# Kernel optimization log

Hardware: AMD Instinct MI355X
Metric: run time of the kernel (lower is better)

The kernel has to match this reference:

```python
import jax, jax.numpy as jnp
import numpy as np

N, L, S, D, H = 4, 8192, 8192, 256, 8
HD = D // H
EPS_ATTN = 1e-6
EPS_LN = 1e-5


def _layer_norm(x, g, b):
    mu = jnp.mean(x, axis=-1, keepdims=True)
    var = jnp.mean((x - mu) ** 2, axis=-1, keepdims=True)
    return (x - mu) / jnp.sqrt(var + EPS_LN) * g + b


def setup_inputs() -> dict:
    key = jax.random.key(0)
    ks = jax.random.split(key, 12)
    sc = 1.0 / np.sqrt(D)
    sc2 = 1.0 / np.sqrt(2 * D)
    return {
        "x": jax.random.normal(ks[0], (N, L, D), jnp.float32),
        "source": jax.random.normal(ks[1], (N, S, D), jnp.float32),
        "x_mask": jnp.ones((N, L), jnp.float32),
        "source_mask": jnp.ones((N, S), jnp.float32),
        "Wq": jax.random.normal(ks[2], (D, D), jnp.float32) * sc,
        "Wk": jax.random.normal(ks[3], (D, D), jnp.float32) * sc,
        "Wv": jax.random.normal(ks[4], (D, D), jnp.float32) * sc,
        "Wm": jax.random.normal(ks[5], (D, D), jnp.float32) * sc,
        "W1": jax.random.normal(ks[6], (2 * D, 2 * D), jnp.float32) * sc2,
        "W2": jax.random.normal(ks[7], (D, 2 * D), jnp.float32) * sc2,
        "g1": jnp.ones((D,), jnp.float32),
        "b1": jnp.zeros((D,), jnp.float32),
        "g2": jnp.ones((D,), jnp.float32),
        "b2": jnp.zeros((D,), jnp.float32),
    }


def reference(x, source, x_mask, source_mask, Wq, Wk, Wv, Wm, W1, W2, g1, b1, g2, b2):
    n = x.shape[0]
    # QKV projections (Linear without bias: y = x @ W.T), split into heads
    q = (x @ Wq.T).reshape(n, -1, H, HD)         # [N, L, H, HD]
    k = (source @ Wk.T).reshape(n, -1, H, HD)    # [N, S, H, HD]
    v = (source @ Wv.T).reshape(n, -1, H, HD)    # [N, S, H, HD]

    # kernelized linear attention: phi(x) = elu(x) + 1
    Q = jax.nn.elu(q) + 1.0
    K = jax.nn.elu(k) + 1.0
    Q = Q * x_mask[:, :, None, None]
    K = K * source_mask[:, :, None, None]
    v = v * source_mask[:, :, None, None]

    s_len = v.shape[1]
    v = v / s_len
    KV = jnp.einsum('nshd,nshv->nhdv', K, v)                       # [N, H, HD, HD]
    Z = 1.0 / (jnp.einsum('nlhd,nhd->nlh', Q, K.sum(axis=1)) + EPS_ATTN)
    msg = jnp.einsum('nlhd,nhdv,nlh->nlhv', Q, KV, Z) * s_len      # [N, L, H, HD]

    # merge heads + LN
    msg = msg.reshape(n, -1, H * HD) @ Wm.T
    msg = _layer_norm(msg, g1, b1)

    # concat-MLP + LN + residual
    h = jnp.concatenate([x, msg], axis=2) @ W1.T
    h = jax.nn.relu(h) @ W2.T
    h = _layer_norm(h, g2, b2)
    return x + h
```

## Files before the change

### kernel.cpp

```cpp
#include <hip/hip_runtime.h>

using short8 = __attribute__((ext_vector_type(8))) short;
using f32x4  = __attribute__((ext_vector_type(4))) float;

__device__ __forceinline__ float bf2f(unsigned short u) {
  union { unsigned int i; float f; } c; c.i = ((unsigned int)u) << 16; return c.f;
}
__device__ __forceinline__ unsigned short f2bf(float x) {
  union { float f; unsigned int i; } c; c.f = x;
  unsigned int r = c.i + 0x7fffu + ((c.i >> 16) & 1u);
  return (unsigned short)(r >> 16);
}

__global__ void cast_all(const float* __restrict__ x, const float* __restrict__ src,
                         const float* __restrict__ wq, const float* __restrict__ wk,
                         const float* __restrict__ wv, const float* __restrict__ wm,
                         const float* __restrict__ w1, const float* __restrict__ w2,
                         unsigned short* __restrict__ xb, unsigned short* __restrict__ sb,
                         unsigned short* __restrict__ Wb) {
  const int NV = 2097152;
  int stride = gridDim.x * blockDim.x;
  for (int i = blockIdx.x * blockDim.x + threadIdx.x; i < 2 * NV + 163840; i += stride) {
    const float4* s; ushort4* d; int j;
    if (i < NV)            { s = (const float4*)x;   d = (ushort4*)xb; j = i; }
    else if (i < 2 * NV)   { s = (const float4*)src; d = (ushort4*)sb; j = i - NV; }
    else {
      j = i - 2 * NV;
      d = (ushort4*)Wb;
      const float* w;
      int off;
      if      (j < 16384)  { w = wq; off = j; }
      else if (j < 32768)  { w = wk; off = j - 16384; }
      else if (j < 49152)  { w = wv; off = j - 32768; }
      else if (j < 65536)  { w = wm; off = j - 49152; }
      else if (j < 131072) { w = w1; off = j - 65536; }
      else                 { w = w2; off = j - 131072; }
      float4 v = ((const float4*)w)[off];
      ushort4 o; o.x = f2bf(v.x); o.y = f2bf(v.y); o.z = f2bf(v.z); o.w = f2bf(v.w);
      d[j] = o;
      continue;
    }
    float4 v = s[j];
    ushort4 o; o.x = f2bf(v.x); o.y = f2bf(v.y); o.z = f2bf(v.z); o.w = f2bf(v.w);
    d[j] = o;
  }
}

enum { EPI_ELU1_MASK = 1, EPI_KV = 2, EPI_RELU_BF16 = 3 };

template<int EPI, bool SPLITA>
__global__ __launch_bounds__(256)
void gemm_nt(const unsigned short* __restrict__ A, const unsigned short* __restrict__ A2,
             const unsigned short* __restrict__ B,
             void* __restrict__ C0, void* __restrict__ C1, const float* __restrict__ aux,
             int M, int O, int K, float scale) {
  __shared__ unsigned short As[128 * 64];
  __shared__ unsigned short Bs[128 * 64];
  const int t  = threadIdx.x;
  const int w  = t >> 6, l = t & 63;
  const int wr = w >> 1, wc = w & 1;
  const int lr = l & 15, kg = l >> 4;
  const int brow = blockIdx.x * 128, bcol = blockIdx.y * 128;
  const int rsub = l >> 3;
  const int swz  = 8 * ((l & 7) ^ rsub);

  f32x4 acc[4][4];
  f32x4 zero = {0.f, 0.f, 0.f, 0.f};
  #pragma unroll
  for (int m = 0; m < 4; m++)
    #pragma unroll
    for (int n = 0; n < 4; n++) acc[m][n] = zero;

  for (int k0 = 0; k0 < K; k0 += 64) {
    #pragma unroll
    for (int i = 0; i < 4; i++) {
      int c = w * 4 + i;
      int row = c * 8 + rsub;
      const unsigned short* ga;
      if (SPLITA) {
        const unsigned short* base = (k0 < 256) ? A : A2;
        ga = base + (size_t)(brow + row) * 256 + (k0 & 255) + swz;
      } else {
        ga = A + (size_t)(brow + row) * K + k0 + swz;
      }
      const unsigned short* gb = B + (size_t)(bcol + row) * K + k0 + swz;
      __builtin_amdgcn_global_load_lds((__attribute__((address_space(1))) unsigned int*)ga,
          (__attribute__((address_space(3))) unsigned int*)(As + c * 512), 16, 0, 0);
      __builtin_amdgcn_global_load_lds((__attribute__((address_space(1))) unsigned int*)gb,
          (__attribute__((address_space(3))) unsigned int*)(Bs + c * 512), 16, 0, 0);
    }
    __syncthreads();
    #pragma unroll
    for (int kk = 0; kk < 2; kk++) {
      short8 af[4], bfr[4];
      #pragma unroll
      for (int m = 0; m < 4; m++) {
        int r = wr * 64 + m * 16 + lr;
        int cb = kk * 64 + kg * 16;
        af[m] = *(const short8*)((const char*)As + r * 128 + (cb ^ ((r & 7) << 4)));
      }
      #pragma unroll
      for (int n = 0; n < 4; n++) {
        int r = wc * 64 + n * 16 + lr;
        int cb = kk * 64 + kg * 16;
        bfr[n] = *(const short8*)((const char*)Bs + r * 128 + (cb ^ ((r & 7) << 4)));
      }
      #pragma unroll
      for (int m = 0; m < 4; m++)
        #pragma unroll
        for (int n = 0; n < 4; n++)
          acc[m][n] = __builtin_amdgcn_mfma_f32_16x16x32_bf16(af[m], bfr[n], acc[m][n], 0, 0, 0);
    }
    __syncthreads();
  }

  #pragma unroll
  for (int m = 0; m < 4; m++) {
    #pragma unroll
    for (int n = 0; n < 4; n++) {
      int col = bcol + wc * 64 + n * 16 + lr;
      #pragma unroll
      for (int j = 0; j < 4; j++) {
        int row = brow + wr * 64 + m * 16 + kg * 4 + j;
        float v = acc[m][n][j];
        if (EPI == EPI_ELU1_MASK) {
          float e = v > 0.f ? v + 1.f : __expf(v);
          ((unsigned short*)C0)[(size_t)row * O + col] = f2bf(e * aux[row]);
        } else if (EPI == EPI_KV) {
          int colm = col & 255;
          if (col < 256) {
            float e = v > 0.f ? v + 1.f : __expf(v);
            ((unsigned short*)C0)[(size_t)row * 256 + colm] = f2bf(e * aux[row]);
          } else {
            ((unsigned short*)C1)[(size_t)row * 256 + colm] = f2bf(v * aux[row] * scale);
          }
        } else {
          ((unsigned short*)C0)[(size_t)row * O + col] = f2bf(v > 0.f ? v : 0.f);
        }
      }
    }
  }
}

template<int MODE>
__global__ __launch_bounds__(512)
void gemm_ln(const unsigned short* __restrict__ A, const unsigned short* __restrict__ B,
             void* __restrict__ Cout, const float* __restrict__ g, const float* __restrict__ b,
             const float* __restrict__ xres, int K) {
  __shared__ unsigned short As[128 * 64];
  __shared__ unsigned short Bs[256 * 64];
  __shared__ float lnsum[128][4];
  __shared__ float lnsq[128][4];
  const int t  = threadIdx.x;
  const int w  = t >> 6, l = t & 63;
  const int wr = w >> 2, wc = w & 3;
  const int lr = l & 15, kg = l >> 4;
  const int brow = blockIdx.x * 128;
  const int rsub = l >> 3;
  const int swz  = 8 * ((l & 7) ^ rsub);

  f32x4 acc[4][4];
  f32x4 zero = {0.f, 0.f, 0.f, 0.f};
  #pragma unroll
  for (int m = 0; m < 4; m++)
    #pragma unroll
    for (int n = 0; n < 4; n++) acc[m][n] = zero;

  for (int k0 = 0; k0 < K; k0 += 64) {
    #pragma unroll
    for (int i = 0; i < 6; i++) {
      int c = w * 6 + i;
      if (c < 16) {
        int row = c * 8 + rsub;
        const unsigned short* ga = A + (size_t)(brow + row) * K + k0 + swz;
        __builtin_amdgcn_global_load_lds((__attribute__((address_space(1))) unsigned int*)ga,
            (__attribute__((address_space(3))) unsigned int*)(As + c * 512), 16, 0, 0);
      } else {
        int row = (c - 16) * 8 + rsub;
        const unsigned short* gb = B + (size_t)row * K + k0 + swz;
        __builtin_amdgcn_global_load_lds((__attribute__((address_space(1))) unsigned int*)gb,
            (__attribute__((address_space(3))) unsigned int*)(Bs + (c - 16) * 512), 16, 0, 0);
      }
    }
    __syncthreads();
    #pragma unroll
    for (int kk = 0; kk < 2; kk++) {
      short8 af[4], bfr[4];
      #pragma unroll
      for (int m = 0; m < 4; m++) {
        int r = wr * 64 + m * 16 + lr;
        int cb = kk * 64 + kg * 16;
        af[m] = *(const short8*)((const char*)As + r * 128 + (cb ^ ((r & 7) << 4)));
      }
      #pragma unroll
      for (int n = 0; n < 4; n++) {
        int r = wc * 64 + n * 16 + lr;
        int cb = kk * 64 + kg * 16;
        bfr[n] = *(const short8*)((const char*)Bs + r * 128 + (cb ^ ((r & 7) << 4)));
      }
      #pragma unroll
      for (int m = 0; m < 4; m++)
        #pragma unroll
        for (int n = 0; n < 4; n++)
          acc[m][n] = __builtin_amdgcn_mfma_f32_16x16x32_bf16(af[m], bfr[n], acc[m][n], 0, 0, 0);
    }
    __syncthreads();
  }

  #pragma unroll
  for (int m = 0; m < 4; m++) {
    #pragma unroll
    for (int j = 0; j < 4; j++) {
      int rl = wr * 64 + m * 16 + kg * 4 + j;
      float s = 0.f, qq = 0.f;
      #pragma unroll
      for (int n = 0; n < 4; n++) { float v = acc[m][n][j]; s += v; qq += v * v; }
      #pragma unroll
      for (int off = 1; off < 16; off <<= 1) {
        s  += __shfl_xor(s, off, 64);
        qq += __shfl_xor(qq, off, 64);
      }
      if (lr == 0) { lnsum[rl][wc] = s; lnsq[rl][wc] = qq; }
    }
  }
  __syncthreads();

  float gl[4], bl[4];
  #pragma unroll
  for (int n = 0; n < 4; n++) {
    int col = wc * 64 + n * 16 + lr;
    gl[n] = g[col]; bl[n] = b[col];
  }
  #pragma unroll
  for (int m = 0; m < 4; m++) {
    #pragma unroll
    for (int j = 0; j < 4; j++) {
      int rl = wr * 64 + m * 16 + kg * 4 + j;
      float s  = lnsum[rl][0] + lnsum[rl][1] + lnsum[rl][2] + lnsum[rl][3];
      float qq = lnsq[rl][0] + lnsq[rl][1] + lnsq[rl][2] + lnsq[rl][3];
      float mu = s * (1.f / 256.f);
      float var = qq * (1.f / 256.f) - mu * mu;
      float rs = rsqrtf(var + 1e-5f);
      size_t row = (size_t)brow + rl;
      #pragma unroll
      for (int n = 0; n < 4; n++) {
        int col = wc * 64 + n * 16 + lr;
        float y = (acc[m][n][j] - mu) * rs * gl[n] + bl[n];
        if (MODE == 0) ((unsigned short*)Cout)[row * 256 + col] = f2bf(y);
        else           ((float*)Cout)[row * 256 + col] = xres[row * 256 + col] + y;
      }
    }
  }
}

__global__ __launch_bounds__(1024)
void kv_partial(const unsigned short* __restrict__ Kb, const unsigned short* __restrict__ Vb,
                float* __restrict__ part_kv, float* __restrict__ part_ks) {
  __shared__ float Ks[16][256];
  __shared__ float Vs[16][256];
  const int t   = threadIdx.x;
  const int blk = blockIdx.x;
  const int n   = blk >> 6;
  const int s0  = (blk & 63) * 128;
  const int h   = t >> 7, g = (t >> 5) & 3, dv = t & 31;
  const int r16 = t >> 6, c4 = (t & 63) * 4;
  const int cbase = h * 32;
  f32x4 acc0 = {0.f, 0.f, 0.f, 0.f}, acc1 = {0.f, 0.f, 0.f, 0.f};
  float ks = 0.f;

  for (int tile = 0; tile < 8; ++tile) {
    int s = s0 + tile * 16;
    size_t gbase = ((size_t)(n * 8192 + s + r16)) * 256 + c4;
    ushort4 kk = *(const ushort4*)&Kb[gbase];
    ushort4 vv = *(const ushort4*)&Vb[gbase];
    __syncthreads();
    float4 kf; kf.x = bf2f(kk.x); kf.y = bf2f(kk.y); kf.z = bf2f(kk.z); kf.w = bf2f(kk.w);
    float4 vf; vf.x = bf2f(vv.x); vf.y = bf2f(vv.y); vf.z = bf2f(vv.z); vf.w = bf2f(vv.w);
    *(float4*)&Ks[r16][c4] = kf;
    *(float4*)&Vs[r16][c4] = vf;
    __syncthreads();
    if (t < 256) {
      #pragma unroll
      for (int r = 0; r < 16; ++r) ks += Ks[r][t];
    }
    #pragma unroll
    for (int si = 0; si < 16; ++si) {
      f32x4 k0 = *(const f32x4*)&Ks[si][cbase + g * 8];
      f32x4 k1 = *(const f32x4*)&Ks[si][cbase + g * 8 + 4];
      float vx = Vs[si][cbase + dv];
      acc0 += k0 * vx;
      acc1 += k1 * vx;
    }
  }
  float* dst = &part_kv[(size_t)blk * 8192 + h * 1024 + dv * 32 + g * 8];
  *(float4*)(dst + 0) = *(float4*)&acc0;
  *(float4*)(dst + 4) = *(float4*)&acc1;
  if (t < 256) part_ks[blk * 256 + t] = ks;
}

__global__ __launch_bounds__(1024)
void kv_finalize(const float* __restrict__ part_kv, const float* __restrict__ part_ks,
                 float* __restrict__ KVt, float* __restrict__ Ksum) {
  const int b = blockIdx.x, t = threadIdx.x;
  if (b < 32) {
    int n = b >> 3;
    int e = (b & 7) * 1024 + t;
    const float* p = part_kv + (size_t)n * 64 * 8192 + e;
    float s = 0.f;
    #pragma unroll 8
    for (int c = 0; c < 64; ++c) s += p[(size_t)c * 8192];
    KVt[(size_t)n * 8192 + e] = s;
  } else {
    int n = b - 32;
    if (t < 256) {
      const float* p = part_ks + n * 64 * 256 + t;
      float s = 0.f;
      #pragma unroll 8
      for (int c = 0; c < 64; ++c) s += p[c * 256];
      Ksum[n * 256 + t] = s;
    }
  }
}

__global__ __launch_bounds__(256)
void msg_apply(const unsigned short* __restrict__ Qb, const float* __restrict__ KVt,
               const float* __restrict__ Ksum, unsigned short* __restrict__ Mb) {
  __shared__ float KVs[8192];
  __shared__ float Kss[256];
  const int t = threadIdx.x;
  const int row0 = blockIdx.x * 32;
  const int n = blockIdx.x >> 8;
  const int r = t >> 3, h = t & 7;
  for (int i = t; i < 8192; i += 256) {
    int j = i ^ (((i >> 10) & 7) << 2);
    KVs[j] = KVt[(size_t)n * 8192 + i];
  }
  Kss[t] = Ksum[n * 256 + t];
  __syncthreads();

  const unsigned short* qp = &Qb[(size_t)(row0 + r) * 256 + h * 32];
  float q[32];
  #pragma unroll
  for (int i = 0; i < 4; ++i) {
    short8 v = *(const short8*)(qp + i * 8);
    #pragma unroll
    for (int j = 0; j < 8; ++j) q[i * 8 + j] = bf2f((unsigned short)v[j]);
  }
  float zden = 0.f;
  #pragma unroll
  for (int sl = 0; sl < 8; ++sl) {
    f32x4 kv = *(const f32x4*)&Kss[h * 32 + sl * 4];
    zden += q[sl*4+0]*kv[0] + q[sl*4+1]*kv[1] + q[sl*4+2]*kv[2] + q[sl*4+3]*kv[3];
  }
  float z = 8192.f / (zden + 1e-6f);
  const int kvbase = h * 1024;
  short8 ov[4];
  #pragma unroll
  for (int dv = 0; dv < 32; ++dv) {
    float o = 0.f;
    #pragma unroll
    for (int sl = 0; sl < 8; ++sl) {
      f32x4 kv = *(const f32x4*)&KVs[kvbase + dv * 32 + ((sl ^ h) << 2)];
      o += q[sl*4+0]*kv[0] + q[sl*4+1]*kv[1] + q[sl*4+2]*kv[2] + q[sl*4+3]*kv[3];
    }
    ov[dv >> 3][dv & 7] = (short)f2bf(o * z);
  }
  unsigned short* op = (unsigned short*)&Mb[(size_t)(row0 + r) * 256 + h * 32];
  #pragma unroll
  for (int i = 0; i < 4; ++i) *(short8*)(op + i * 8) = ov[i];
}

extern "C" void kernel_launch(void* const* d_in, const int* in_sizes, int n_in,
                              void* d_out, int out_size, void* d_ws, size_t ws_size,
                              hipStream_t stream) {
  const float* x   = (const float*)d_in[0];
  const float* src = (const float*)d_in[1];
  const float* xm  = (const float*)d_in[2];
  const float* sm  = (const float*)d_in[3];
  const float* Wq  = (const float*)d_in[4];
  const float* Wk  = (const float*)d_in[5];
  const float* Wv  = (const float*)d_in[6];
  const float* Wm  = (const float*)d_in[7];
  const float* W1  = (const float*)d_in[8];
  const float* W2  = (const float*)d_in[9];
  const float* g1  = (const float*)d_in[10];
  const float* b1  = (const float*)d_in[11];
  const float* g2  = (const float*)d_in[12];
  const float* b2  = (const float*)d_in[13];
  float* out = (float*)d_out;
  char*  ws  = (char*)d_ws;

  unsigned short* xb   = (unsigned short*)(ws);
  unsigned short* sb   = (unsigned short*)(ws + 16777216);
  unsigned short* Qb   = (unsigned short*)(ws + 33554432);
  unsigned short* Mb   = (unsigned short*)(ws + 50331648);
  unsigned short* Kb   = (unsigned short*)(ws + 67108864);
  unsigned short* Vb   = (unsigned short*)(ws + 83886080);
  float*          pkv  = (float*)(ws + 16777216);
  float*          pks  = (float*)(ws + 16777216 + 8388608);
  unsigned short* msgb = (unsigned short*)(ws + 67108864);
  unsigned short* h1b  = (unsigned short*)(ws + 33554432);
  float*          KV   = (float*)(ws + 100663296);
  float*          Ksm  = (float*)(ws + 100663296 + 131072);
  unsigned short* Wb   = (unsigned short*)(ws + 100663296 + 135168);
  unsigned short* Wqb = Wb;
  unsigned short* Wkb = Wb + 65536;
  unsigned short* Wmb = Wb + 196608;
  unsigned short* W1b = Wb + 262144;
  unsigned short* W2b = Wb + 524288;

  cast_all<<<4096, 256, 0, stream>>>(x, src, Wq, Wk, Wv, Wm, W1, W2, xb, sb, Wb);

  gemm_nt<EPI_ELU1_MASK, false><<<dim3(256, 2), 256, 0, stream>>>(
      xb, nullptr, Wqb, (void*)Qb, nullptr, xm, 32768, 256, 256, 0.f);
  gemm_nt<EPI_KV, false><<<dim3(256, 4), 256, 0, stream>>>(
      sb, nullptr, Wkb, (void*)Kb, (void*)Vb, sm, 32768, 512, 256, 1.f / 8192.f);

  kv_partial<<<256, 1024, 0, stream>>>(Kb, Vb, pkv, pks);
  kv_finalize<<<36, 1024, 0, stream>>>(pkv, pks, KV, Ksm);
  msg_apply<<<1024, 256, 0, stream>>>(Qb, KV, Ksm, Mb);

  gemm_ln<0><<<256, 512, 0, stream>>>(Mb, Wmb, (void*)msgb, g1, b1, nullptr, 256);

  gemm_nt<EPI_RELU_BF16, true><<<dim3(256, 4), 256, 0, stream>>>(
      xb, msgb, W1b, (void*)h1b, nullptr, nullptr, 32768, 512, 512, 0.f);

  gemm_ln<1><<<256, 512, 0, stream>>>(h1b, W2b, (void*)out, g2, b2, x, 512);
}
```

Measured before the change: 286.5 us.

## Merge Q and KV projection GEMMs and double-buffer LDS tiles

Combines the Q projection and the K/V projection into a single GEMM launch with a six-column-tile grid, choosing x or source as the A operand per column block and writing Q, K, V in the epilogue. Adds double-buffered shared memory so the next K-slice is prefetched asynchronously while MFMAs run on the current one. This aims to cut launch overhead and tail effects and to hide global load latency, at the cost of doubling LDS use, which may lower occupancy.

```diff
diff --git a/kernel.cpp b/kernel.cpp
--- a/kernel.cpp
+++ b/kernel.cpp
@@ -46,16 +46,17 @@
   }
 }
 
-enum { EPI_ELU1_MASK = 1, EPI_KV = 2, EPI_RELU_BF16 = 3 };
-
-template<int EPI, bool SPLITA>
+enum { EPI_QKV = 0, EPI_RELU_BF16 = 1 };
+
+template<int EPI, int ASEL>
 __global__ __launch_bounds__(256)
 void gemm_nt(const unsigned short* __restrict__ A, const unsigned short* __restrict__ A2,
              const unsigned short* __restrict__ B,
-             void* __restrict__ C0, void* __restrict__ C1, const float* __restrict__ aux,
+             void* __restrict__ C0, void* __restrict__ C1, void* __restrict__ C2,
+             const float* __restrict__ aux0, const float* __restrict__ aux1,
              int M, int O, int K, float scale) {
-  __shared__ unsigned short As[128 * 64];
-  __shared__ unsigned short Bs[128 * 64];
+  __shared__ unsigned short As[2][128 * 64];
+  __shared__ unsigned short Bs[2][128 * 64];
   const int t  = threadIdx.x;
   const int w  = t >> 6, l = t & 63;
   const int wr = w >> 1, wc = w & 1;
@@ -64,6 +65,8 @@
   const int rsub = l >> 3;
   const int swz  = 8 * ((l & 7) ^ rsub);
 
+  const unsigned short* Ablk = (ASEL == 2 && bcol >= 256) ? A2 : A;
+
   f32x4 acc[4][4];
   f32x4 zero = {0.f, 0.f, 0.f, 0.f};
   #pragma unroll
@@ -71,25 +74,31 @@
     #pragma unroll
     for (int n = 0; n < 4; n++) acc[m][n] = zero;
 
-  for (int k0 = 0; k0 < K; k0 += 64) {
+  auto STAGE = [&](int bufi, int k0s) {
     #pragma unroll
     for (int i = 0; i < 4; i++) {
       int c = w * 4 + i;
       int row = c * 8 + rsub;
       const unsigned short* ga;
-      if (SPLITA) {
-        const unsigned short* base = (k0 < 256) ? A : A2;
-        ga = base + (size_t)(brow + row) * 256 + (k0 & 255) + swz;
+      if (ASEL == 1) {
+        const unsigned short* base = (k0s < 256) ? A : A2;
+        ga = base + (size_t)(brow + row) * 256 + (k0s & 255) + swz;
       } else {
-        ga = A + (size_t)(brow + row) * K + k0 + swz;
-      }
-      const unsigned short* gb = B + (size_t)(bcol + row) * K + k0 + swz;
+        ga = Ablk + (size_t)(brow + row) * K + k0s + swz;
+      }
+      const unsigned short* gb = B + (size_t)(bcol + row) * K + k0s + swz;
       __builtin_amdgcn_global_load_lds((__attribute__((address_space(1))) unsigned int*)ga,
-          (__attribute__((address_space(3))) unsigned int*)(As + c * 512), 16, 0, 0);
+          (__attribute__((address_space(3))) unsigned int*)(&As[bufi][0] + c * 512), 16, 0, 0);
       __builtin_amdgcn_global_load_lds((__attribute__((address_space(1))) unsigned int*)gb,
-          (__attribute__((address_space(3))) unsigned int*)(Bs + c * 512), 16, 0, 0);
-    }
-    __syncthreads();
+          (__attribute__((address_space(3))) unsigned int*)(&Bs[bufi][0] + c * 512), 16, 0, 0);
+    }
+  };
+
+  STAGE(0, 0);
+  __syncthreads();
+  int cur = 0;
+  for (int k0 = 0; k0 < K; k0 += 64) {
+    if (k0 + 64 < K) STAGE(cur ^ 1, k0 + 64);
     #pragma unroll
     for (int kk = 0; kk < 2; kk++) {
       short8 af[4], bfr[4];
@@ -97,13 +106,13 @@
       for (int m = 0; m < 4; m++) {
         int r = wr * 64 + m * 16 + lr;
         int cb = kk * 64 + kg * 16;
-        af[m] = *(const short8*)((const char*)As + r * 128 + (cb ^ ((r & 7) << 4)));
+        af[m] = *(const short8*)((const char*)&As[cur][0] + r * 128 + (cb ^ ((r & 7) << 4)));
       }
       #pragma unroll
       for (int n = 0; n < 4; n++) {
         int r = wc * 64 + n * 16 + lr;
         int cb = kk * 64 + kg * 16;
-        bfr[n] = *(const short8*)((const char*)Bs + r * 128 + (cb ^ ((r & 7) << 4)));
+        bfr[n] = *(const short8*)((const char*)&Bs[cur][0] + r * 128 + (cb ^ ((r & 7) << 4)));
       }
       #pragma unroll
       for (int m = 0; m < 4; m++)
@@ -112,6 +121,7 @@
           acc[m][n] = __builtin_amdgcn_mfma_f32_16x16x32_bf16(af[m], bfr[n], acc[m][n], 0, 0, 0);
     }
     __syncthreads();
+    cur ^= 1;
   }
 
   #pragma unroll
@@ -123,16 +133,15 @@
       for (int j = 0; j < 4; j++) {
         int row = brow + wr * 64 + m * 16 + kg * 4 + j;
         float v = acc[m][n][j];
-        if (EPI == EPI_ELU1_MASK) {
-          float e = v > 0.f ? v + 1.f : __expf(v);
-          ((unsigned short*)C0)[(size_t)row * O + col] = f2bf(e * aux[row]);
-        } else if (EPI == EPI_KV) {
-          int colm = col & 255;
+        if (EPI == EPI_QKV) {
           if (col < 256) {
             float e = v > 0.f ? v + 1.f : __expf(v);
-            ((unsigned short*)C0)[(size_t)row * 256 + colm] = f2bf(e * aux[row]);
+            ((unsigned short*)C0)[(size_t)row * 256 + col] = f2bf(e * aux0[row]);
+          } else if (col < 512) {
+            float e = v > 0.f ? v + 1.f : __expf(v);
+            ((unsigned short*)C1)[(size_t)row * 256 + (col - 256)] = f2bf(e * aux1[row]);
           } else {
-            ((unsigned short*)C1)[(size_t)row * 256 + colm] = f2bf(v * aux[row] * scale);
+            ((unsigned short*)C2)[(size_t)row * 256 + (col - 512)] = f2bf(v * aux1[row] * scale);
           }
         } else {
           ((unsigned short*)C0)[(size_t)row * O + col] = f2bf(v > 0.f ? v : 0.f);
@@ -404,17 +413,14 @@
   float*          Ksm  = (float*)(ws + 100663296 + 131072);
   unsigned short* Wb   = (unsigned short*)(ws + 100663296 + 135168);
   unsigned short* Wqb = Wb;
-  unsigned short* Wkb = Wb + 65536;
   unsigned short* Wmb = Wb + 196608;
   unsigned short* W1b = Wb + 262144;
   unsigned short* W2b = Wb + 524288;
 
   cast_all<<<4096, 256, 0, stream>>>(x, src, Wq, Wk, Wv, Wm, W1, W2, xb, sb, Wb);
 
-  gemm_nt<EPI_ELU1_MASK, false><<<dim3(256, 2), 256, 0, stream>>>(
-      xb, nullptr, Wqb, (void*)Qb, nullptr, xm, 32768, 256, 256, 0.f);
-  gemm_nt<EPI_KV, false><<<dim3(256, 4), 256, 0, stream>>>(
-      sb, nullptr, Wkb, (void*)Kb, (void*)Vb, sm, 32768, 512, 256, 1.f / 8192.f);
+  gemm_nt<EPI_QKV, 2><<<dim3(256, 6), 256, 0, stream>>>(
+      xb, sb, Wqb, (void*)Qb, (void*)Kb, (void*)Vb, xm, sm, 32768, 768, 256, 1.f / 8192.f);
 
   kv_partial<<<256, 1024, 0, stream>>>(Kb, Vb, pkv, pks);
   kv_finalize<<<36, 1024, 0, stream>>>(pkv, pks, KV, Ksm);
@@ -422,8 +428,8 @@
 
   gemm_ln<0><<<256, 512, 0, stream>>>(Mb, Wmb, (void*)msgb, g1, b1, nullptr, 256);
 
-  gemm_nt<EPI_RELU_BF16, true><<<dim3(256, 4), 256, 0, stream>>>(
-      xb, msgb, W1b, (void*)h1b, nullptr, nullptr, 32768, 512, 512, 0.f);
+  gemm_nt<EPI_RELU_BF16, 1><<<dim3(256, 4), 256, 0, stream>>>(
+      xb, msgb, W1b, (void*)h1b, nullptr, nullptr, nullptr, nullptr, 32768, 512, 512, 0.f);
 
   gemm_ln<1><<<256, 512, 0, stream>>>(h1b, W2b, (void*)out, g2, b2, x, 512);
 }
```

New measurement: 299.3 us. +4.5%, slower.

## Merge Q and KV projections into one launch with wider 128x256 tiles

Applied to the files above, without the earlier changes.

The separate Q and K/V projection GEMMs become one launch with three 256-column panels: the Q panel reads x and the K and V panels read source. The GEMM kernel moves to 512 threads and 128x256 output tiles, for both the QKV and the W1 ReLU GEMM, so each A tile is reused across twice as many output columns. This removes one launch and halves redundant A-tile loads, at the cost of more LDS per block and fewer blocks, which may reduce occupancy.

```diff
diff --git a/kernel.cpp b/kernel.cpp
--- a/kernel.cpp
+++ b/kernel.cpp
@@ -46,24 +46,29 @@
   }
 }
 
-enum { EPI_ELU1_MASK = 1, EPI_KV = 2, EPI_RELU_BF16 = 3 };
-
-template<int EPI, bool SPLITA>
-__global__ __launch_bounds__(256)
-void gemm_nt(const unsigned short* __restrict__ A, const unsigned short* __restrict__ A2,
-             const unsigned short* __restrict__ B,
-             void* __restrict__ C0, void* __restrict__ C1, const float* __restrict__ aux,
-             int M, int O, int K, float scale) {
+enum { EPI_QKV = 0, EPI_RELU = 1 };
+
+template<int EPI>
+__global__ __launch_bounds__(512)
+void gemm8(const unsigned short* __restrict__ A, const unsigned short* __restrict__ A2,
+           const unsigned short* __restrict__ B,
+           void* __restrict__ C0, void* __restrict__ C1, void* __restrict__ C2,
+           const float* __restrict__ aux0, const float* __restrict__ aux1,
+           int K, float scale) {
   __shared__ unsigned short As[128 * 64];
-  __shared__ unsigned short Bs[128 * 64];
+  __shared__ unsigned short Bs[256 * 64];
   const int t  = threadIdx.x;
   const int w  = t >> 6, l = t & 63;
-  const int wr = w >> 1, wc = w & 1;
+  const int wr = w >> 2, wc = w & 3;
   const int lr = l & 15, kg = l >> 4;
-  const int brow = blockIdx.x * 128, bcol = blockIdx.y * 128;
+  const int brow = blockIdx.x * 128;
+  const int panel = blockIdx.y;
   const int rsub = l >> 3;
   const int swz  = 8 * ((l & 7) ^ rsub);
 
+  const unsigned short* Aq = (EPI == EPI_QKV && panel > 0) ? A2 : A;
+  const unsigned short* Bp = B + (size_t)(panel * 256) * K;
+
   f32x4 acc[4][4];
   f32x4 zero = {0.f, 0.f, 0.f, 0.f};
   #pragma unroll
@@ -73,21 +78,25 @@
 
   for (int k0 = 0; k0 < K; k0 += 64) {
     #pragma unroll
-    for (int i = 0; i < 4; i++) {
-      int c = w * 4 + i;
-      int row = c * 8 + rsub;
-      const unsigned short* ga;
-      if (SPLITA) {
-        const unsigned short* base = (k0 < 256) ? A : A2;
-        ga = base + (size_t)(brow + row) * 256 + (k0 & 255) + swz;
+    for (int i = 0; i < 6; i++) {
+      int c = w * 6 + i;
+      if (c < 16) {
+        int row = c * 8 + rsub;
+        const unsigned short* ga;
+        if (EPI == EPI_RELU) {
+          const unsigned short* base = (k0 < 256) ? A : A2;
+          ga = base + (size_t)(brow + row) * 256 + (k0 & 255) + swz;
+        } else {
+          ga = Aq + (size_t)(brow + row) * K + k0 + swz;
+        }
+        __builtin_amdgcn_global_load_lds((__attribute__((address_space(1))) unsigned int*)ga,
+            (__attribute__((address_space(3))) unsigned int*)(As + c * 512), 16, 0, 0);
       } else {
-        ga = A + (size_t)(brow + row) * K + k0 + swz;
-      }
-      const unsigned short* gb = B + (size_t)(bcol + row) * K + k0 + swz;
-      __builtin_amdgcn_global_load_lds((__attribute__((address_space(1))) unsigned int*)ga,
-          (__attribute__((address_space(3))) unsigned int*)(As + c * 512), 16, 0, 0);
-      __builtin_amdgcn_global_load_lds((__attribute__((address_space(1))) unsigned int*)gb,
-          (__attribute__((address_space(3))) unsigned int*)(Bs + c * 512), 16, 0, 0);
+        int row = (c - 16) * 8 + rsub;
+        const unsigned short* gb = Bp + (size_t)row * K + k0 + swz;
+        __builtin_amdgcn_global_load_lds((__attribute__((address_space(1))) unsigned int*)gb,
+            (__attribute__((address_space(3))) unsigned int*)(Bs + (c - 16) * 512), 16, 0, 0);
+      }
     }
     __syncthreads();
     #pragma unroll
@@ -118,24 +127,23 @@
   for (int m = 0; m < 4; m++) {
     #pragma unroll
     for (int n = 0; n < 4; n++) {
-      int col = bcol + wc * 64 + n * 16 + lr;
+      int col = wc * 64 + n * 16 + lr;
       #pragma unroll
       for (int j = 0; j < 4; j++) {
         int row = brow + wr * 64 + m * 16 + kg * 4 + j;
         float v = acc[m][n][j];
-        if (EPI == EPI_ELU1_MASK) {
-          float e = v > 0.f ? v + 1.f : __expf(v);
-          ((unsigned short*)C0)[(size_t)row * O + col] = f2bf(e * aux[row]);
-        } else if (EPI == EPI_KV) {
-          int colm = col & 255;
-          if (col < 256) {
+        if (EPI == EPI_QKV) {
+          if (panel == 0) {
             float e = v > 0.f ? v + 1.f : __expf(v);
-            ((unsigned short*)C0)[(size_t)row * 256 + colm] = f2bf(e * aux[row]);
+            ((unsigned short*)C0)[(size_t)row * 256 + col] = f2bf(e * aux0[row]);
+          } else if (panel == 1) {
+            float e = v > 0.f ? v + 1.f : __expf(v);
+            ((unsigned short*)C1)[(size_t)row * 256 + col] = f2bf(e * aux1[row]);
           } else {
-            ((unsigned short*)C1)[(size_t)row * 256 + colm] = f2bf(v * aux[row] * scale);
+            ((unsigned short*)C2)[(size_t)row * 256 + col] = f2bf(v * aux1[row] * scale);
           }
         } else {
-          ((unsigned short*)C0)[(size_t)row * O + col] = f2bf(v > 0.f ? v : 0.f);
+          ((unsigned short*)C0)[(size_t)row * 512 + panel * 256 + col] = f2bf(v > 0.f ? v : 0.f);
         }
       }
     }
@@ -404,17 +412,14 @@
   float*          Ksm  = (float*)(ws + 100663296 + 131072);
   unsigned short* Wb   = (unsigned short*)(ws + 100663296 + 135168);
   unsigned short* Wqb = Wb;
-  unsigned short* Wkb = Wb + 65536;
   unsigned short* Wmb = Wb + 196608;
   unsigned short* W1b = Wb + 262144;
   unsigned short* W2b = Wb + 524288;
 
   cast_all<<<4096, 256, 0, stream>>>(x, src, Wq, Wk, Wv, Wm, W1, W2, xb, sb, Wb);
 
-  gemm_nt<EPI_ELU1_MASK, false><<<dim3(256, 2), 256, 0, stream>>>(
-      xb, nullptr, Wqb, (void*)Qb, nullptr, xm, 32768, 256, 256, 0.f);
-  gemm_nt<EPI_KV, false><<<dim3(256, 4), 256, 0, stream>>>(
-      sb, nullptr, Wkb, (void*)Kb, (void*)Vb, sm, 32768, 512, 256, 1.f / 8192.f);
+  gemm8<EPI_QKV><<<dim3(256, 3), 512, 0, stream>>>(
+      xb, sb, Wqb, (void*)Qb, (void*)Kb, (void*)Vb, xm, sm, 256, 1.f / 8192.f);
 
   kv_partial<<<256, 1024, 0, stream>>>(Kb, Vb, pkv, pks);
   kv_finalize<<<36, 1024, 0, stream>>>(pkv, pks, KV, Ksm);
@@ -422,8 +427,8 @@
 
   gemm_ln<0><<<256, 512, 0, stream>>>(Mb, Wmb, (void*)msgb, g1, b1, nullptr, 256);
 
-  gemm_nt<EPI_RELU_BF16, true><<<dim3(256, 4), 256, 0, stream>>>(
-      xb, msgb, W1b, (void*)h1b, nullptr, nullptr, 32768, 512, 512, 0.f);
+  gemm8<EPI_RELU><<<dim3(256, 2), 512, 0, stream>>>(
+      xb, msgb, W1b, (void*)h1b, nullptr, nullptr, nullptr, nullptr, 512, 0.f);
 
   gemm_ln<1><<<256, 512, 0, stream>>>(h1b, W2b, (void*)out, g2, b2, x, 512);
 }
```

New measurement: 306.4 us. 1.07x slower.
